# Kernel tuning notes

Hardware: AMD Instinct MI355X
Metric: run time of the kernel (lower is better)

## Reference

```python
import jax, jax.numpy as jnp
import numpy as np

B, N, F, FH, H = 8, 2048, 64, 64, 4
NEG_BIG = -1e10


def setup_inputs() -> dict:
    key = jax.random.key(0)
    k_x, k_a, k_w, k_as, k_an = jax.random.split(key, 5)
    X = jax.random.normal(k_x, (B, N, F), dtype=jnp.float32)
    A = (jax.random.uniform(k_a, (B, N, N)) < 0.1).astype(jnp.float32)
    A = jnp.maximum(A, jnp.eye(N, dtype=jnp.float32)[None])
    W = jax.random.normal(k_w, (H, F, FH), dtype=jnp.float32) * (1.0 / np.sqrt(F))
    b = jnp.zeros((H, FH), dtype=jnp.float32)
    a_self = jax.random.normal(k_as, (H, FH), dtype=jnp.float32) * (1.0 / np.sqrt(FH))
    a_neigh = jax.random.normal(k_an, (H, FH), dtype=jnp.float32) * (1.0 / np.sqrt(FH))
    return {"X": X, "A": A, "W": W, "b": b, "a_self": a_self, "a_neigh": a_neigh}


def reference(X, A, W, b, a_self, a_neigh):
    # per-head linear projection: [B,H,N,FH]
    feats = jnp.einsum("bnf,hfo->bhno", X, W)
    # additive attention logits: e_ij = leaky_relu(a_s.h_i + a_n.h_j)
    s_self = jnp.einsum("bhno,ho->bhn", feats, a_self)   # [B,H,N]
    s_neigh = jnp.einsum("bhno,ho->bhn", feats, a_neigh)  # [B,H,N]
    scores = s_self[:, :, :, None] + s_neigh[:, :, None, :]  # [B,H,N,N]
    scores = jax.nn.leaky_relu(scores, negative_slope=0.2)
    scores = scores + (1.0 - A)[:, None] * NEG_BIG  # adjacency mask
    attn = jax.nn.softmax(scores, axis=-1)
    # weighted aggregation + bias (dropouts are identity at inference)
    out = jnp.einsum("bhnm,bhmo->bhno", attn, feats) + b[None, :, None, :]
    # concat heads -> [B,N,H*FH], then activation
    Bd, Hd, Nd, Fd = out.shape
    out = jnp.transpose(out, (0, 2, 1, 3)).reshape(Bd, Nd, Hd * Fd)
    return jax.nn.relu(out)
```

## Files before the change

kernel.cpp:

```cpp
#include <hip/hip_runtime.h>
#include <hip/hip_bf16.h>
#include <stdint.h>

#define B_ 8
#define N_ 2048
#define F_ 64
#define FH_ 64
#define H_ 4
#define C_ (H_*FH_)
#define CHUNK 64
#define NCHUNK (N_/CHUNK)
#define LOG2E 1.44269504088896340736f

typedef short short8 __attribute__((ext_vector_type(8)));
typedef float f32x4 __attribute__((ext_vector_type(4)));

__device__ __forceinline__ short f2bf(float f) {
    __hip_bfloat16 h = __float2bfloat16(f);
    return __builtin_bit_cast(short, h);
}

__device__ __forceinline__ void async16(void* l, const void* g) {
    __builtin_amdgcn_global_load_lds((const __attribute__((address_space(1))) unsigned int*)g,
                                     (__attribute__((address_space(3))) unsigned int*)l, 16, 0, 0);
}

__global__ __launch_bounds__(256) void kf(const float* __restrict__ A,
                                          const float* __restrict__ X,
                                          const float* __restrict__ W,
                                          const float* __restrict__ a_self,
                                          const float* __restrict__ a_neigh,
                                          unsigned long long* __restrict__ Amask,
                                          __hip_bfloat16* __restrict__ featsT,
                                          float* __restrict__ ss,
                                          float* __restrict__ sn) {
    __shared__ float a_lds[2][FH_];
    __shared__ __hip_bfloat16 cw_lds[FH_ * 72];
    const int bx = blockIdx.x;
    const int tid = threadIdx.x;
    const int wave = tid >> 6, lane = tid & 63;

    if (bx >= 1024) {
        const int R = (bx - 1024) * 4 + wave;
        const float* arow = A + (size_t)R * N_;
        unsigned long long* mrow = Amask + (size_t)R * (N_ / 64);
#pragma unroll
        for (int i = 0; i < 8; ++i) {
            float a0 = arow[i * 256 + lane];
            float a1 = arow[i * 256 + 64 + lane];
            float a2 = arow[i * 256 + 128 + lane];
            float a3 = arow[i * 256 + 192 + lane];
            unsigned long long m0 = __ballot(a0 != 0.0f);
            unsigned long long m1 = __ballot(a1 != 0.0f);
            unsigned long long m2 = __ballot(a2 != 0.0f);
            unsigned long long m3 = __ballot(a3 != 0.0f);
            if (lane == 0) {
                mrow[i * 4 + 0] = m0; mrow[i * 4 + 1] = m1;
                mrow[i * 4 + 2] = m2; mrow[i * 4 + 3] = m3;
            }
        }
        return;
    }

    const int nb = bx & 31, h = (bx >> 5) & 3, b = bx >> 7;

    if (tid < 64)       a_lds[0][tid] = a_self[h * FH_ + tid];
    else if (tid < 128) a_lds[1][tid - 64] = a_neigh[h * FH_ + tid - 64];
    {
        int f = tid >> 2, o0 = (tid & 3) * 16;
        const float* wsrc = W + ((size_t)(h * F_ + f)) * FH_ + o0;
#pragma unroll
        for (int k = 0; k < 16; ++k)
            cw_lds[(o0 + k) * 72 + f] = __float2bfloat16(wsrc[k]);
    }
    __syncthreads();

    const int m = lane & 15, q = lane >> 4;
    const int nl = wave * 16 + m;
    const int n = nb * 64 + nl;
    f32x4 acc[4] = {};
#pragma unroll
    for (int ks = 0; ks < 2; ++ks) {
        const float* xp = X + ((size_t)(b * N_ + n)) * F_ + ks * 32 + q * 8;
        float4 x0 = *(const float4*)xp;
        float4 x1 = *(const float4*)(xp + 4);
        short8 bfrag;
        bfrag[0] = f2bf(x0.x); bfrag[1] = f2bf(x0.y);
        bfrag[2] = f2bf(x0.z); bfrag[3] = f2bf(x0.w);
        bfrag[4] = f2bf(x1.x); bfrag[5] = f2bf(x1.y);
        bfrag[6] = f2bf(x1.z); bfrag[7] = f2bf(x1.w);
#pragma unroll
        for (int ot = 0; ot < 4; ++ot) {
            short8 afrag = *(const short8*)(cw_lds + (ot * 16 + m) * 72 + ks * 32 + q * 8);
            acc[ot] = __builtin_amdgcn_mfma_f32_16x16x32_bf16(afrag, bfrag, acc[ot], 0, 0, 0);
        }
    }
    __syncthreads();
    float ssv = 0.f, snv = 0.f;
#pragma unroll
    for (int ot = 0; ot < 4; ++ot) {
#pragma unroll
        for (int r = 0; r < 4; ++r) {
            int orow = ot * 16 + q * 4 + r;
            float v = acc[ot][r];
            cw_lds[orow * 72 + nl] = __float2bfloat16(v);
            ssv += v * a_lds[0][orow];
            snv += v * a_lds[1][orow];
        }
    }
    ssv += __shfl_xor(ssv, 16); ssv += __shfl_xor(ssv, 32);
    snv += __shfl_xor(snv, 16); snv += __shfl_xor(snv, 32);
    __syncthreads();
    {
        int o = tid >> 2, c = (tid & 3) * 16;
        const __hip_bfloat16* src = cw_lds + o * 72 + c;
        __hip_bfloat16* dst = featsT + ((size_t)(b * H_ + h) * FH_ + o) * N_ + nb * 64 + c;
        *(uint4*)dst       = *(const uint4*)src;
        *(uint4*)(dst + 8) = *(const uint4*)(src + 8);
    }
    if (lane < 16) {
        size_t idx = ((size_t)(b * H_ + h)) * N_ + n;
        ss[idx] = ssv * LOG2E;
        sn[idx] = snv * LOG2E;
    }
}

__global__ __launch_bounds__(256, 4) void k3_attn(const unsigned int* __restrict__ Amask,
                                                  const __hip_bfloat16* __restrict__ featsT,
                                                  const float* __restrict__ ss,
                                                  const float* __restrict__ sn,
                                                  const float* __restrict__ bias,
                                                  float* __restrict__ out) {
    __shared__ __hip_bfloat16 fv_lds[2][64 * CHUNK];
    __shared__ float e1_lds[N_];
    __shared__ float e2_lds[N_];

    const int tile = blockIdx.x, h = blockIdx.y, b = blockIdx.z;
    const int tid = threadIdx.x, wave = tid >> 6, lane = tid & 63;
    const int m = lane & 15, q = lane >> 4;
    const int rowtile = tile * 64;

    {
        const float4* snrow = (const float4*)(sn + ((size_t)(b * H_ + h)) * N_);
        float4* e1v = (float4*)e1_lds;
        float4* e2v = (float4*)e2_lds;
#pragma unroll
        for (int i = 0; i < 2; ++i) {
            int idx = tid + i * 256;
            float4 v = snrow[idx];
            float4 u1, u2;
            u1.x = exp2f(v.x); u1.y = exp2f(v.y); u1.z = exp2f(v.z); u1.w = exp2f(v.w);
            u2.x = exp2f(0.2f * v.x); u2.y = exp2f(0.2f * v.y);
            u2.z = exp2f(0.2f * v.z); u2.w = exp2f(0.2f * v.w);
            e1v[idx] = u1; e2v[idx] = u2;
        }
    }
    const float ssi = ss[((size_t)(b * H_ + h)) * N_ + rowtile + wave * 16 + m];
    const float e1i = exp2f(ssi), e2i = exp2f(0.2f * ssi);

    const __hip_bfloat16* fhead = featsT + ((size_t)(b * H_ + h)) * FH_ * N_;
    const unsigned int* mrow = Amask + ((size_t)(b * N_) + rowtile + wave * 16 + m) * (N_ / 32);

    auto stage = [&](int c, int bufi) {
        const int cb = c * CHUNK;
#pragma unroll
        for (int i = 0; i < 2; ++i) {
            int base_unit = i * 256 + wave * 64;
            int unit = base_unit + lane;
            int o = unit >> 3, v = unit & 7;
            int u = v ^ (o & 7);
            async16(&fv_lds[bufi][base_unit * 8], fhead + (size_t)o * N_ + cb + u * 8);
        }
    };

    auto buildP = [&](int c, unsigned int mA, unsigned int mB, short8& pA, short8& pB) {
        const int cg = c * CHUNK;
        float4 eA10 = *(const float4*)(e1_lds + cg + q * 8);
        float4 eA11 = *(const float4*)(e1_lds + cg + q * 8 + 4);
        float4 eB10 = *(const float4*)(e1_lds + cg + 32 + q * 8);
        float4 eB11 = *(const float4*)(e1_lds + cg + 32 + q * 8 + 4);
        float4 eA20 = *(const float4*)(e2_lds + cg + q * 8);
        float4 eA21 = *(const float4*)(e2_lds + cg + q * 8 + 4);
        float4 eB20 = *(const float4*)(e2_lds + cg + 32 + q * 8);
        float4 eB21 = *(const float4*)(e2_lds + cg + 32 + q * 8 + 4);
        float e1A[8] = {eA10.x, eA10.y, eA10.z, eA10.w, eA11.x, eA11.y, eA11.z, eA11.w};
        float e1B[8] = {eB10.x, eB10.y, eB10.z, eB10.w, eB11.x, eB11.y, eB11.z, eB11.w};
        float e2A[8] = {eA20.x, eA20.y, eA20.z, eA20.w, eA21.x, eA21.y, eA21.z, eA21.w};
        float e2B[8] = {eB20.x, eB20.y, eB20.z, eB20.w, eB21.x, eB21.y, eB21.z, eB21.w};
#pragma unroll
        for (int s = 0; s < 8; ++s) {
            float vA = fmaxf(e1i * e1A[s], e2i * e2A[s]);
            float vB = fmaxf(e1i * e1B[s], e2i * e2B[s]);
            const int bit = q * 8 + s;
            pA[s] = (mA >> bit) & 1 ? f2bf(vA) : (short)0;
            pB[s] = (mB >> bit) & 1 ? f2bf(vB) : (short)0;
        }
    };

    uint2 mk_use = *(const uint2*)(mrow + 0);
    uint2 mk_a   = *(const uint2*)(mrow + 2);

    stage(0, 0);
    __syncthreads();

    f32x4 acc[2][4] = {};
    f32x4 accl[2] = {};
    short8 ones;
#pragma unroll
    for (int s = 0; s < 8; ++s) ones[s] = (short)0x3F80;

    short8 pA, pB;
    buildP(0, mk_use.x, mk_use.y, pA, pB);

    for (int c = 0; c < NCHUNK; ++c) {
        const int cur = c & 1;
        if (c + 1 < NCHUNK) stage(c + 1, cur ^ 1);
        uint2 mk_b = mk_a;
        if (c + 2 < NCHUNK) mk_b = *(const uint2*)(mrow + (c + 2) * 2);

        short8 fA[4], fB[4];
#pragma unroll
        for (int ct = 0; ct < 4; ++ct) {
            int o = ct * 16 + m;
            fA[ct] = *(const short8*)(fv_lds[cur] + ((o << 3) + (q ^ (o & 7))) * 8);
            fB[ct] = *(const short8*)(fv_lds[cur] + ((o << 3) + ((4 + q) ^ (o & 7))) * 8);
        }
#pragma unroll
        for (int ct = 0; ct < 4; ++ct) {
            acc[0][ct] = __builtin_amdgcn_mfma_f32_16x16x32_bf16(pA, fA[ct], acc[0][ct], 0, 0, 0);
            acc[1][ct] = __builtin_amdgcn_mfma_f32_16x16x32_bf16(pB, fB[ct], acc[1][ct], 0, 0, 0);
        }
        accl[0] = __builtin_amdgcn_mfma_f32_16x16x32_bf16(pA, ones, accl[0], 0, 0, 0);
        accl[1] = __builtin_amdgcn_mfma_f32_16x16x32_bf16(pB, ones, accl[1], 0, 0, 0);

        if (c + 1 < NCHUNK) buildP(c + 1, mk_a.x, mk_a.y, pA, pB);
        mk_a = mk_b;

        __syncthreads();
    }

    float bc[4];
#pragma unroll
    for (int ct = 0; ct < 4; ++ct) bc[ct] = bias[h * FH_ + ct * 16 + m];

#pragma unroll
    for (int r = 0; r < 4; ++r) {
        float inv = 1.0f / (accl[0][r] + accl[1][r]);
        int gr = rowtile + wave * 16 + q * 4 + r;
#pragma unroll
        for (int ct = 0; ct < 4; ++ct) {
            float v = (acc[0][ct][r] + acc[1][ct][r]) * inv + bc[ct];
            out[((size_t)(b * N_) + gr) * C_ + h * FH_ + ct * 16 + m] = fmaxf(v, 0.0f);
        }
    }
}

extern "C" void kernel_launch(void* const* d_in, const int* in_sizes, int n_in,
                              void* d_out, int out_size, void* d_ws, size_t ws_size,
                              hipStream_t stream) {
    const float* X       = (const float*)d_in[0];
    const float* A       = (const float*)d_in[1];
    const float* W       = (const float*)d_in[2];
    const float* bias    = (const float*)d_in[3];
    const float* a_self  = (const float*)d_in[4];
    const float* a_neigh = (const float*)d_in[5];
    float* out = (float*)d_out;

    char* ws = (char*)d_ws;
    __hip_bfloat16* featsT = (__hip_bfloat16*)(ws);
    float* ss              = (float*)(ws + 8421376);
    float* sn              = (float*)(ws + 8683520);
    unsigned long long* Am = (unsigned long long*)(ws + 8945664);

    kf      <<<5120, 256, 0, stream>>>(A, X, W, a_self, a_neigh, Am, featsT, ss, sn);
    k3_attn <<<dim3(N_ / 64, H_, B_), 256, 0, stream>>>((const unsigned int*)Am, featsT, ss, sn, bias, out);
}
```

Measured before the change: 249.5 us.

## Read features directly from global and compute two row-tiles per wave

The attention kernel drops the double-buffered LDS staging of the transposed feature chunk and its per-chunk block barrier, loading the MFMA B-operands straight from global memory. Each wave now handles 32 rows (two 16-row groups), so every feature fragment it loads feeds twice as many MFMAs, and the grid shrinks by half. This removes the __syncthreads from the main loop and the LDS traffic, but relies on L1/L2 to serve the repeated feature reads across waves and blocks. It also raises register pressure and drops the occupancy hint from launch bounds.

```diff
diff --git a/kernel.cpp b/kernel.cpp
--- a/kernel.cpp
+++ b/kernel.cpp
@@ -18,11 +18,6 @@
 __device__ __forceinline__ short f2bf(float f) {
     __hip_bfloat16 h = __float2bfloat16(f);
     return __builtin_bit_cast(short, h);
-}
-
-__device__ __forceinline__ void async16(void* l, const void* g) {
-    __builtin_amdgcn_global_load_lds((const __attribute__((address_space(1))) unsigned int*)g,
-                                     (__attribute__((address_space(3))) unsigned int*)l, 16, 0, 0);
 }
 
 __global__ __launch_bounds__(256) void kf(const float* __restrict__ A,
@@ -125,20 +120,19 @@
     }
 }
 
-__global__ __launch_bounds__(256, 4) void k3_attn(const unsigned int* __restrict__ Amask,
-                                                  const __hip_bfloat16* __restrict__ featsT,
-                                                  const float* __restrict__ ss,
-                                                  const float* __restrict__ sn,
-                                                  const float* __restrict__ bias,
-                                                  float* __restrict__ out) {
-    __shared__ __hip_bfloat16 fv_lds[2][64 * CHUNK];
+__global__ __launch_bounds__(256) void k3_attn(const unsigned int* __restrict__ Amask,
+                                               const __hip_bfloat16* __restrict__ featsT,
+                                               const float* __restrict__ ss,
+                                               const float* __restrict__ sn,
+                                               const float* __restrict__ bias,
+                                               float* __restrict__ out) {
     __shared__ float e1_lds[N_];
     __shared__ float e2_lds[N_];
 
     const int tile = blockIdx.x, h = blockIdx.y, b = blockIdx.z;
     const int tid = threadIdx.x, wave = tid >> 6, lane = tid & 63;
     const int m = lane & 15, q = lane >> 4;
-    const int rowtile = tile * 64;
+    const int wavebase = tile * 128 + wave * 32;
 
     {
         const float4* snrow = (const float4*)(sn + ((size_t)(b * H_ + h)) * N_);
@@ -155,26 +149,42 @@
             e1v[idx] = u1; e2v[idx] = u2;
         }
     }
-    const float ssi = ss[((size_t)(b * H_ + h)) * N_ + rowtile + wave * 16 + m];
-    const float e1i = exp2f(ssi), e2i = exp2f(0.2f * ssi);
+    const float* ssrow = ss + ((size_t)(b * H_ + h)) * N_;
+    const float ssi0 = ssrow[wavebase + m];
+    const float ssi1 = ssrow[wavebase + 16 + m];
+    const float e1i0 = exp2f(ssi0), e2i0 = exp2f(0.2f * ssi0);
+    const float e1i1 = exp2f(ssi1), e2i1 = exp2f(0.2f * ssi1);
 
     const __hip_bfloat16* fhead = featsT + ((size_t)(b * H_ + h)) * FH_ * N_;
-    const unsigned int* mrow = Amask + ((size_t)(b * N_) + rowtile + wave * 16 + m) * (N_ / 32);
-
-    auto stage = [&](int c, int bufi) {
-        const int cb = c * CHUNK;
-#pragma unroll
-        for (int i = 0; i < 2; ++i) {
-            int base_unit = i * 256 + wave * 64;
-            int unit = base_unit + lane;
-            int o = unit >> 3, v = unit & 7;
-            int u = v ^ (o & 7);
-            async16(&fv_lds[bufi][base_unit * 8], fhead + (size_t)o * N_ + cb + u * 8);
-        }
-    };
-
-    auto buildP = [&](int c, unsigned int mA, unsigned int mB, short8& pA, short8& pB) {
+    const unsigned int* mrow0 = Amask + ((size_t)(b * N_) + wavebase + m) * (N_ / 32);
+    const unsigned int* mrow1 = mrow0 + (size_t)16 * (N_ / 32);
+
+    __syncthreads();
+
+    f32x4 acc[2][4] = {};
+    f32x4 accl[2] = {};
+    short8 ones;
+#pragma unroll
+    for (int s = 0; s < 8; ++s) ones[s] = (short)0x3F80;
+
+    uint2 mk0 = *(const uint2*)(mrow0);
+    uint2 mk1 = *(const uint2*)(mrow1);
+
+    for (int c = 0; c < NCHUNK; ++c) {
         const int cg = c * CHUNK;
+        short8 fA[4], fB[4];
+#pragma unroll
+        for (int ct = 0; ct < 4; ++ct) {
+            const __hip_bfloat16* fp = fhead + (size_t)(ct * 16 + m) * N_ + cg + q * 8;
+            fA[ct] = *(const short8*)fp;
+            fB[ct] = *(const short8*)(fp + 32);
+        }
+        uint2 mk0n = mk0, mk1n = mk1;
+        if (c + 1 < NCHUNK) {
+            mk0n = *(const uint2*)(mrow0 + (c + 1) * 2);
+            mk1n = *(const uint2*)(mrow1 + (c + 1) * 2);
+        }
+
         float4 eA10 = *(const float4*)(e1_lds + cg + q * 8);
         float4 eA11 = *(const float4*)(e1_lds + cg + q * 8 + 4);
         float4 eB10 = *(const float4*)(e1_lds + cg + 32 + q * 8);
@@ -187,56 +197,33 @@
         float e1B[8] = {eB10.x, eB10.y, eB10.z, eB10.w, eB11.x, eB11.y, eB11.z, eB11.w};
         float e2A[8] = {eA20.x, eA20.y, eA20.z, eA20.w, eA21.x, eA21.y, eA21.z, eA21.w};
         float e2B[8] = {eB20.x, eB20.y, eB20.z, eB20.w, eB21.x, eB21.y, eB21.z, eB21.w};
+
+        short8 p0A, p0B, p1A, p1B;
 #pragma unroll
         for (int s = 0; s < 8; ++s) {
-            float vA = fmaxf(e1i * e1A[s], e2i * e2A[s]);
-            float vB = fmaxf(e1i * e1B[s], e2i * e2B[s]);
+            float vA0 = fmaxf(e1i0 * e1A[s], e2i0 * e2A[s]);
+            float vB0 = fmaxf(e1i0 * e1B[s], e2i0 * e2B[s]);
+            float vA1 = fmaxf(e1i1 * e1A[s], e2i1 * e2A[s]);
+            float vB1 = fmaxf(e1i1 * e1B[s], e2i1 * e2B[s]);
             const int bit = q * 8 + s;
-            pA[s] = (mA >> bit) & 1 ? f2bf(vA) : (short)0;
-            pB[s] = (mB >> bit) & 1 ? f2bf(vB) : (short)0;
-        }
-    };
-
-    uint2 mk_use = *(const uint2*)(mrow + 0);
-    uint2 mk_a   = *(const uint2*)(mrow + 2);
-
-    stage(0, 0);
-    __syncthreads();
-
-    f32x4 acc[2][4] = {};
-    f32x4 accl[2] = {};
-    short8 ones;
-#pragma unroll
-    for (int s = 0; s < 8; ++s) ones[s] = (short)0x3F80;
-
-    short8 pA, pB;
-    buildP(0, mk_use.x, mk_use.y, pA, pB);
-
-    for (int c = 0; c < NCHUNK; ++c) {
-        const int cur = c & 1;
-        if (c + 1 < NCHUNK) stage(c + 1, cur ^ 1);
-        uint2 mk_b = mk_a;
-        if (c + 2 < NCHUNK) mk_b = *(const uint2*)(mrow + (c + 2) * 2);
-
-        short8 fA[4], fB[4];
+            p0A[s] = (mk0.x >> bit) & 1 ? f2bf(vA0) : (short)0;
+            p0B[s] = (mk0.y >> bit) & 1 ? f2bf(vB0) : (short)0;
+            p1A[s] = (mk1.x >> bit) & 1 ? f2bf(vA1) : (short)0;
+            p1B[s] = (mk1.y >> bit) & 1 ? f2bf(vB1) : (short)0;
+        }
 #pragma unroll
         for (int ct = 0; ct < 4; ++ct) {
-            int o = ct * 16 + m;
-            fA[ct] = *(const short8*)(fv_lds[cur] + ((o << 3) + (q ^ (o & 7))) * 8);
-            fB[ct] = *(const short8*)(fv_lds[cur] + ((o << 3) + ((4 + q) ^ (o & 7))) * 8);
-        }
-#pragma unroll
-        for (int ct = 0; ct < 4; ++ct) {
-            acc[0][ct] = __builtin_amdgcn_mfma_f32_16x16x32_bf16(pA, fA[ct], acc[0][ct], 0, 0, 0);
-            acc[1][ct] = __builtin_amdgcn_mfma_f32_16x16x32_bf16(pB, fB[ct], acc[1][ct], 0, 0, 0);
-        }
-        accl[0] = __builtin_amdgcn_mfma_f32_16x16x32_bf16(pA, ones, accl[0], 0, 0, 0);
-        accl[1] = __builtin_amdgcn_mfma_f32_16x16x32_bf16(pB, ones, accl[1], 0, 0, 0);
-
-        if (c + 1 < NCHUNK) buildP(c + 1, mk_a.x, mk_a.y, pA, pB);
-        mk_a = mk_b;
-
-        __syncthreads();
+            acc[0][ct] = __builtin_amdgcn_mfma_f32_16x16x32_bf16(p0A, fA[ct], acc[0][ct], 0, 0, 0);
+            acc[0][ct] = __builtin_amdgcn_mfma_f32_16x16x32_bf16(p0B, fB[ct], acc[0][ct], 0, 0, 0);
+            acc[1][ct] = __builtin_amdgcn_mfma_f32_16x16x32_bf16(p1A, fA[ct], acc[1][ct], 0, 0, 0);
+            acc[1][ct] = __builtin_amdgcn_mfma_f32_16x16x32_bf16(p1B, fB[ct], acc[1][ct], 0, 0, 0);
+        }
+        accl[0] = __builtin_amdgcn_mfma_f32_16x16x32_bf16(p0A, ones, accl[0], 0, 0, 0);
+        accl[0] = __builtin_amdgcn_mfma_f32_16x16x32_bf16(p0B, ones, accl[0], 0, 0, 0);
+        accl[1] = __builtin_amdgcn_mfma_f32_16x16x32_bf16(p1A, ones, accl[1], 0, 0, 0);
+        accl[1] = __builtin_amdgcn_mfma_f32_16x16x32_bf16(p1B, ones, accl[1], 0, 0, 0);
+
+        mk0 = mk0n; mk1 = mk1n;
     }
 
     float bc[4];
@@ -244,13 +231,16 @@
     for (int ct = 0; ct < 4; ++ct) bc[ct] = bias[h * FH_ + ct * 16 + m];
 
 #pragma unroll
-    for (int r = 0; r < 4; ++r) {
-        float inv = 1.0f / (accl[0][r] + accl[1][r]);
-        int gr = rowtile + wave * 16 + q * 4 + r;
-#pragma unroll
-        for (int ct = 0; ct < 4; ++ct) {
-            float v = (acc[0][ct][r] + acc[1][ct][r]) * inv + bc[ct];
-            out[((size_t)(b * N_) + gr) * C_ + h * FH_ + ct * 16 + m] = fmaxf(v, 0.0f);
+    for (int g = 0; g < 2; ++g) {
+#pragma unroll
+        for (int r = 0; r < 4; ++r) {
+            float inv = 1.0f / accl[g][r];
+            int gr = wavebase + g * 16 + q * 4 + r;
+#pragma unroll
+            for (int ct = 0; ct < 4; ++ct) {
+                float v = acc[g][ct][r] * inv + bc[ct];
+                out[((size_t)(b * N_) + gr) * C_ + h * FH_ + ct * 16 + m] = fmaxf(v, 0.0f);
+            }
         }
     }
 }
@@ -273,5 +263,5 @@
     unsigned long long* Am = (unsigned long long*)(ws + 8945664);
 
     kf      <<<5120, 256, 0, stream>>>(A, X, W, a_self, a_neigh, Am, featsT, ss, sn);
-    k3_attn <<<dim3(N_ / 64, H_, B_), 256, 0, stream>>>((const unsigned int*)Am, featsT, ss, sn, bias, out);
-}
+    k3_attn <<<dim3(N_ / 128, H_, B_), 256, 0, stream>>>((const unsigned int*)Am, featsT, ss, sn, bias, out);
+}
```

Result: slower. 282.7 us (+13.3%).

## Process two 16-row groups per wave to reuse staged feature chunks

Applied to the files above, without the earlier changes.

Each wave now handles 32 query rows (two 16-row groups) instead of 16, so each block covers 128 rows and the grid is halved. The feature fragments loaded from LDS and the exponentiated neighbour-score table are shared across both row groups, cutting global staging and LDS traffic per row. The software-pipelined P construction for the next chunk is removed in favour of building P inline each iteration. This doubles accumulator registers and halves block count, which may reduce occupancy and the overlap between ALU and MFMA work.

```diff
diff --git a/kernel.cpp b/kernel.cpp
--- a/kernel.cpp
+++ b/kernel.cpp
@@ -138,7 +138,7 @@
     const int tile = blockIdx.x, h = blockIdx.y, b = blockIdx.z;
     const int tid = threadIdx.x, wave = tid >> 6, lane = tid & 63;
     const int m = lane & 15, q = lane >> 4;
-    const int rowtile = tile * 64;
+    const int wrow = tile * 128 + wave * 32;
 
     {
         const float4* snrow = (const float4*)(sn + ((size_t)(b * H_ + h)) * N_);
@@ -155,11 +155,15 @@
             e1v[idx] = u1; e2v[idx] = u2;
         }
     }
-    const float ssi = ss[((size_t)(b * H_ + h)) * N_ + rowtile + wave * 16 + m];
-    const float e1i = exp2f(ssi), e2i = exp2f(0.2f * ssi);
+    const float* ssrow = ss + ((size_t)(b * H_ + h)) * N_;
+    const float ssi0 = ssrow[wrow + m];
+    const float ssi1 = ssrow[wrow + 16 + m];
+    const float e1i0 = exp2f(ssi0), e2i0 = exp2f(0.2f * ssi0);
+    const float e1i1 = exp2f(ssi1), e2i1 = exp2f(0.2f * ssi1);
 
     const __hip_bfloat16* fhead = featsT + ((size_t)(b * H_ + h)) * FH_ * N_;
-    const unsigned int* mrow = Amask + ((size_t)(b * N_) + rowtile + wave * 16 + m) * (N_ / 32);
+    const unsigned int* mrow0 = Amask + ((size_t)(b * N_) + wrow + m) * (N_ / 32);
+    const unsigned int* mrow1 = mrow0 + (size_t)16 * (N_ / 32);
 
     auto stage = [&](int c, int bufi) {
         const int cb = c * CHUNK;
@@ -173,7 +177,27 @@
         }
     };
 
-    auto buildP = [&](int c, unsigned int mA, unsigned int mB, short8& pA, short8& pB) {
+    uint2 mk0 = *(const uint2*)(mrow0);
+    uint2 mk1 = *(const uint2*)(mrow1);
+
+    stage(0, 0);
+    __syncthreads();
+
+    f32x4 acc[2][4] = {};
+    f32x4 accl[2] = {};
+    short8 ones;
+#pragma unroll
+    for (int t = 0; t < 8; ++t) ones[t] = (short)0x3F80;
+
+    for (int c = 0; c < NCHUNK; ++c) {
+        const int cur = c & 1;
+        if (c + 1 < NCHUNK) stage(c + 1, cur ^ 1);
+        uint2 mk0n = mk0, mk1n = mk1;
+        if (c + 1 < NCHUNK) {
+            mk0n = *(const uint2*)(mrow0 + (c + 1) * 2);
+            mk1n = *(const uint2*)(mrow1 + (c + 1) * 2);
+        }
+
         const int cg = c * CHUNK;
         float4 eA10 = *(const float4*)(e1_lds + cg + q * 8);
         float4 eA11 = *(const float4*)(e1_lds + cg + q * 8 + 4);
@@ -187,36 +211,6 @@
         float e1B[8] = {eB10.x, eB10.y, eB10.z, eB10.w, eB11.x, eB11.y, eB11.z, eB11.w};
         float e2A[8] = {eA20.x, eA20.y, eA20.z, eA20.w, eA21.x, eA21.y, eA21.z, eA21.w};
         float e2B[8] = {eB20.x, eB20.y, eB20.z, eB20.w, eB21.x, eB21.y, eB21.z, eB21.w};
-#pragma unroll
-        for (int s = 0; s < 8; ++s) {
-            float vA = fmaxf(e1i * e1A[s], e2i * e2A[s]);
-            float vB = fmaxf(e1i * e1B[s], e2i * e2B[s]);
-            const int bit = q * 8 + s;
-            pA[s] = (mA >> bit) & 1 ? f2bf(vA) : (short)0;
-            pB[s] = (mB >> bit) & 1 ? f2bf(vB) : (short)0;
-        }
-    };
-
-    uint2 mk_use = *(const uint2*)(mrow + 0);
-    uint2 mk_a   = *(const uint2*)(mrow + 2);
-
-    stage(0, 0);
-    __syncthreads();
-
-    f32x4 acc[2][4] = {};
-    f32x4 accl[2] = {};
-    short8 ones;
-#pragma unroll
-    for (int s = 0; s < 8; ++s) ones[s] = (short)0x3F80;
-
-    short8 pA, pB;
-    buildP(0, mk_use.x, mk_use.y, pA, pB);
-
-    for (int c = 0; c < NCHUNK; ++c) {
-        const int cur = c & 1;
-        if (c + 1 < NCHUNK) stage(c + 1, cur ^ 1);
-        uint2 mk_b = mk_a;
-        if (c + 2 < NCHUNK) mk_b = *(const uint2*)(mrow + (c + 2) * 2);
 
         short8 fA[4], fB[4];
 #pragma unroll
@@ -225,17 +219,45 @@
             fA[ct] = *(const short8*)(fv_lds[cur] + ((o << 3) + (q ^ (o & 7))) * 8);
             fB[ct] = *(const short8*)(fv_lds[cur] + ((o << 3) + ((4 + q) ^ (o & 7))) * 8);
         }
-#pragma unroll
-        for (int ct = 0; ct < 4; ++ct) {
-            acc[0][ct] = __builtin_amdgcn_mfma_f32_16x16x32_bf16(pA, fA[ct], acc[0][ct], 0, 0, 0);
-            acc[1][ct] = __builtin_amdgcn_mfma_f32_16x16x32_bf16(pB, fB[ct], acc[1][ct], 0, 0, 0);
-        }
-        accl[0] = __builtin_amdgcn_mfma_f32_16x16x32_bf16(pA, ones, accl[0], 0, 0, 0);
-        accl[1] = __builtin_amdgcn_mfma_f32_16x16x32_bf16(pB, ones, accl[1], 0, 0, 0);
-
-        if (c + 1 < NCHUNK) buildP(c + 1, mk_a.x, mk_a.y, pA, pB);
-        mk_a = mk_b;
-
+
+        {
+            short8 pA, pB;
+#pragma unroll
+            for (int t = 0; t < 8; ++t) {
+                float vA = fmaxf(e1i0 * e1A[t], e2i0 * e2A[t]);
+                float vB = fmaxf(e1i0 * e1B[t], e2i0 * e2B[t]);
+                const int bit = q * 8 + t;
+                pA[t] = (mk0.x >> bit) & 1 ? f2bf(vA) : (short)0;
+                pB[t] = (mk0.y >> bit) & 1 ? f2bf(vB) : (short)0;
+            }
+#pragma unroll
+            for (int ct = 0; ct < 4; ++ct) {
+                acc[0][ct] = __builtin_amdgcn_mfma_f32_16x16x32_bf16(pA, fA[ct], acc[0][ct], 0, 0, 0);
+                acc[0][ct] = __builtin_amdgcn_mfma_f32_16x16x32_bf16(pB, fB[ct], acc[0][ct], 0, 0, 0);
+            }
+            accl[0] = __builtin_amdgcn_mfma_f32_16x16x32_bf16(pA, ones, accl[0], 0, 0, 0);
+            accl[0] = __builtin_amdgcn_mfma_f32_16x16x32_bf16(pB, ones, accl[0], 0, 0, 0);
+        }
+        {
+            short8 pA, pB;
+#pragma unroll
+            for (int t = 0; t < 8; ++t) {
+                float vA = fmaxf(e1i1 * e1A[t], e2i1 * e2A[t]);
+                float vB = fmaxf(e1i1 * e1B[t], e2i1 * e2B[t]);
+                const int bit = q * 8 + t;
+                pA[t] = (mk1.x >> bit) & 1 ? f2bf(vA) : (short)0;
+                pB[t] = (mk1.y >> bit) & 1 ? f2bf(vB) : (short)0;
+            }
+#pragma unroll
+            for (int ct = 0; ct < 4; ++ct) {
+                acc[1][ct] = __builtin_amdgcn_mfma_f32_16x16x32_bf16(pA, fA[ct], acc[1][ct], 0, 0, 0);
+                acc[1][ct] = __builtin_amdgcn_mfma_f32_16x16x32_bf16(pB, fB[ct], acc[1][ct], 0, 0, 0);
+            }
+            accl[1] = __builtin_amdgcn_mfma_f32_16x16x32_bf16(pA, ones, accl[1], 0, 0, 0);
+            accl[1] = __builtin_amdgcn_mfma_f32_16x16x32_bf16(pB, ones, accl[1], 0, 0, 0);
+        }
+
+        mk0 = mk0n; mk1 = mk1n;
         __syncthreads();
     }
 
@@ -244,13 +266,16 @@
     for (int ct = 0; ct < 4; ++ct) bc[ct] = bias[h * FH_ + ct * 16 + m];
 
 #pragma unroll
-    for (int r = 0; r < 4; ++r) {
-        float inv = 1.0f / (accl[0][r] + accl[1][r]);
-        int gr = rowtile + wave * 16 + q * 4 + r;
-#pragma unroll
-        for (int ct = 0; ct < 4; ++ct) {
-            float v = (acc[0][ct][r] + acc[1][ct][r]) * inv + bc[ct];
-            out[((size_t)(b * N_) + gr) * C_ + h * FH_ + ct * 16 + m] = fmaxf(v, 0.0f);
+    for (int g = 0; g < 2; ++g) {
+#pragma unroll
+        for (int r = 0; r < 4; ++r) {
+            float inv = 1.0f / accl[g][r];
+            int gr = wrow + g * 16 + q * 4 + r;
+#pragma unroll
+            for (int ct = 0; ct < 4; ++ct) {
+                float v = acc[g][ct][r] * inv + bc[ct];
+                out[((size_t)(b * N_) + gr) * C_ + h * FH_ + ct * 16 + m] = fmaxf(v, 0.0f);
+            }
         }
     }
 }
@@ -273,5 +298,5 @@
     unsigned long long* Am = (unsigned long long*)(ws + 8945664);
 
     kf      <<<5120, 256, 0, stream>>>(A, X, W, a_self, a_neigh, Am, featsT, ss, sn);
-    k3_attn <<<dim3(N_ / 64, H_, B_), 256, 0, stream>>>((const unsigned int*)Am, featsT, ss, sn, bias, out);
-}
+    k3_attn <<<dim3(N_ / 128, H_, B_), 256, 0, stream>>>((const unsigned int*)Am, featsT, ss, sn, bias, out);
+}
```

Result: slower. 297.0 us (+19.0%).
